# Kernel optimization log

Hardware: AMD Instinct MI355X
Metric: run time of the kernel (lower is better)

Reference implementation:

```python
import jax, jax.numpy as jnp
import numpy as np

DIM = 512
HEADS = 8
DIM_HEAD = 64
CROSS_DIM = 768
FF_INNER = 4 * DIM  # 2048
SCALE = DIM_HEAD ** -0.5
EPS = 1e-5


def _layer_norm(x, g, b):
    mu = jnp.mean(x, axis=-1, keepdims=True)
    var = jnp.var(x, axis=-1, keepdims=True)
    return (x - mu) * jax.lax.rsqrt(var + EPS) * g + b


def _mha(q, k, v):
    # q: [B,Sq,D], k/v: [B,Sk,D] -> [B,Sq,D]
    B, Sq, D = q.shape
    Sk = k.shape[1]
    qh = q.reshape(B, Sq, HEADS, DIM_HEAD).transpose(0, 2, 1, 3)
    kh = k.reshape(B, Sk, HEADS, DIM_HEAD).transpose(0, 2, 1, 3)
    vh = v.reshape(B, Sk, HEADS, DIM_HEAD).transpose(0, 2, 1, 3)
    scores = jnp.einsum('bhqd,bhkd->bhqk', qh, kh) * SCALE
    probs = jax.nn.softmax(scores, axis=-1)
    out = jnp.einsum('bhqk,bhkd->bhqd', probs, vh)
    return out.transpose(0, 2, 1, 3).reshape(B, Sq, D)


def setup_inputs() -> dict:
    key = jax.random.key(0)
    ks = jax.random.split(key, 20)
    s = 0.02
    inp = {
        'x': jax.random.normal(ks[0], (8, 1024, DIM), jnp.float32),
        'enc': jax.random.normal(ks[1], (8, 77, CROSS_DIM), jnp.float32),
        # self-attention (attn1)
        'ln1_g': jnp.ones((DIM,), jnp.float32),
        'ln1_b': jnp.zeros((DIM,), jnp.float32),
        'wq1': jax.random.normal(ks[2], (DIM, DIM), jnp.float32) * s,
        'wk1': jax.random.normal(ks[3], (DIM, DIM), jnp.float32) * s,
        'wv1': jax.random.normal(ks[4], (DIM, DIM), jnp.float32) * s,
        'wo1': jax.random.normal(ks[5], (DIM, DIM), jnp.float32) * s,
        'bo1': jnp.zeros((DIM,), jnp.float32),
        # cross-attention (attn2)
        'ln2_g': jnp.ones((DIM,), jnp.float32),
        'ln2_b': jnp.zeros((DIM,), jnp.float32),
        'wq2': jax.random.normal(ks[6], (DIM, DIM), jnp.float32) * s,
        'wk2': jax.random.normal(ks[7], (CROSS_DIM, DIM), jnp.float32) * s,
        'wv2': jax.random.normal(ks[8], (CROSS_DIM, DIM), jnp.float32) * s,
        'wo2': jax.random.normal(ks[9], (DIM, DIM), jnp.float32) * s,
        'bo2': jnp.zeros((DIM,), jnp.float32),
        # feed-forward (GEGLU)
        'ln3_g': jnp.ones((DIM,), jnp.float32),
        'ln3_b': jnp.zeros((DIM,), jnp.float32),
        'wg': jax.random.normal(ks[10], (DIM, 2 * FF_INNER), jnp.float32) * s,
        'bg': jnp.zeros((2 * FF_INNER,), jnp.float32),
        'wf': jax.random.normal(ks[11], (FF_INNER, DIM), jnp.float32) * s,
        'bf': jnp.zeros((DIM,), jnp.float32),
    }
    return inp


def reference(x, enc, ln1_g, ln1_b, wq1, wk1, wv1, wo1, bo1,
              ln2_g, ln2_b, wq2, wk2, wv2, wo2, bo2,
              ln3_g, ln3_b, wg, bg, wf, bf):
    # self-attention block (pre-norm)
    h = _layer_norm(x, ln1_g, ln1_b)
    a = _mha(h @ wq1, h @ wk1, h @ wv1)
    x = x + a @ wo1 + bo1
    # cross-attention block (pre-norm)
    h = _layer_norm(x, ln2_g, ln2_b)
    a = _mha(h @ wq2, enc @ wk2, enc @ wv2)
    x = x + a @ wo2 + bo2
    # GEGLU feed-forward (pre-norm)
    h = _layer_norm(x, ln3_g, ln3_b)
    proj = h @ wg + bg
    u, g = jnp.split(proj, 2, axis=-1)
    ff = (u * jax.nn.gelu(g, approximate=False)) @ wf + bf
    return x + ff
```

## Files before the change

### kernel.cpp

```cpp
#include <hip/hip_runtime.h>


typedef _Float16 half8 __attribute__((ext_vector_type(8)));
typedef float f32x4 __attribute__((ext_vector_type(4)));

__device__ __forceinline__ f32x4 mfma16(half8 a, half8 b, f32x4 c) {
  return __builtin_amdgcn_mfma_f32_16x16x32_f16(a, b, c, 0, 0, 0);
}

__device__ __forceinline__ void gload16(const _Float16* g, _Float16* l) {
  __builtin_amdgcn_global_load_lds(
      (const __attribute__((address_space(1))) void*)g,
      (__attribute__((address_space(3))) void*)l, 16, 0, 0);
}

struct PrepArgs {
  const float* src[10];
  _Float16* dst[10];
  int K[10], N[10], base[10];
  const float* enc;
  _Float16* ench;
  int encBase, nEnc;
};

__global__ __launch_bounds__(256)
void prep_all(PrepArgs pa) {
  __shared__ float tile[32][33];
  const int bid = blockIdx.x;
  const int tx = threadIdx.x, ty = threadIdx.y;
  if (bid >= pa.encBase) {
    const int i = (bid - pa.encBase) * 256 + ty * 32 + tx;
    if (i < pa.nEnc) pa.ench[i] = (_Float16)pa.enc[i];
    return;
  }
  int mi = 0;
  #pragma unroll
  for (int j = 1; j < 10; j++)
    if (bid >= pa.base[j]) mi = j;
  const int K = pa.K[mi], N = pa.N[mi];
  const int rel = bid - pa.base[mi];
  const int ntiles = N >> 5;
  const int bx = rel % ntiles, by = rel / ntiles;
  const float* src = pa.src[mi];
  _Float16* dst = pa.dst[mi];
  const int n0 = bx * 32, k0 = by * 32;
  #pragma unroll
  for (int j = ty; j < 32; j += 8)
    tile[j][tx] = src[(size_t)(k0 + j) * N + n0 + tx];
  __syncthreads();
  #pragma unroll
  for (int j = ty; j < 32; j += 8)
    dst[(size_t)(n0 + j) * K + k0 + tx] = (_Float16)tile[tx][j];
}

__global__ __launch_bounds__(256)
void vt_kernel(const _Float16* __restrict__ src, _Float16* __restrict__ dst,
               int S, int srcStride, int dstStride) {
  __shared__ _Float16 tile[32][33];
  const int tx = threadIdx.x, ty = threadIdx.y;
  const int s0 = blockIdx.x * 32, d0 = blockIdx.y * 32, bh = blockIdx.z;
  const int b = bh >> 3, h = bh & 7;
  const _Float16* sp = src + (size_t)b * S * srcStride + h * 64 + d0;
  #pragma unroll
  for (int j = ty; j < 32; j += 8) {
    int s = s0 + j; if (s >= S) s = S - 1;
    tile[j][tx] = sp[(size_t)s * srcStride + tx];
  }
  __syncthreads();
  _Float16* dp = dst + ((size_t)bh * 64 + d0) * dstStride + s0;
  #pragma unroll
  for (int j = ty; j < 32; j += 8)
    dp[(size_t)j * dstStride + tx] = tile[tx][j];
}

__global__ __launch_bounds__(256)
void ln_kernel(const float* __restrict__ x, const float* __restrict__ g,
               const float* __restrict__ b, _Float16* __restrict__ out) {
  const int row = blockIdx.x, t = threadIdx.x;
  const float* xr = x + (size_t)row * 512;
  float v0 = xr[t], v1 = xr[t + 256];
  float s1 = v0 + v1, s2 = v0 * v0 + v1 * v1;
  #pragma unroll
  for (int m = 32; m >= 1; m >>= 1) {
    s1 += __shfl_xor(s1, m);
    s2 += __shfl_xor(s2, m);
  }
  __shared__ float red[8];
  if ((t & 63) == 0) { red[t >> 6] = s1; red[4 + (t >> 6)] = s2; }
  __syncthreads();
  s1 = red[0] + red[1] + red[2] + red[3];
  s2 = red[4] + red[5] + red[6] + red[7];
  const float mu = s1 * (1.0f / 512.0f);
  const float var = s2 * (1.0f / 512.0f) - mu * mu;
  const float rs = rsqrtf(var + 1e-5f);
  out[(size_t)row * 512 + t] = (_Float16)((v0 - mu) * rs * g[t] + b[t]);
  out[(size_t)row * 512 + t + 256] =
      (_Float16)((v1 - mu) * rs * g[t + 256] + b[t + 256]);
}

template <int EPI, int GWM, int GWN, int WM, int WN, int MW, int SWZ>
__global__ __launch_bounds__(256, MW)
void gemm_bt(const _Float16* __restrict__ A, const _Float16* __restrict__ BT,
             int M, int N, int K, int lda, int ldc,
             _Float16* Ch, float* Cf,
             const float* __restrict__ bias, const float* resid) {
  constexpr int BM = GWM * WM * 16;
  constexpr int BN = GWN * WN * 16;
  __shared__ __align__(16) _Float16 As[2][4 * BM * 8];
  __shared__ __align__(16) _Float16 Bs[2][4 * BN * 8];
  __shared__ __align__(16) _Float16 Bs2[(EPI == 2) ? 2 : 1]
                                      [(EPI == 2) ? 4 * BN * 8 : 8];

  const int t = threadIdx.x;
  const int NNB = (N + BN - 1) / BN;
  int bm, bn;
  if constexpr (SWZ) {
    const int MG = (M / BM) >> 3;
    const int xcd = blockIdx.x & 7;
    const int s = blockIdx.x >> 3;
    bm = xcd * MG + s % MG;
    bn = s / MG;
  } else {
    bn = blockIdx.x % NNB;
    bm = blockIdx.x / NNB;
  }
  const int m0 = bm * BM, n0 = bn * BN;
  const int lane = t & 63, wv = t >> 6;
  const int quad = lane >> 4, l15 = lane & 15;
  const int wm = wv / GWN, wn = wv % GWN;

  f32x4 zero4 = {0.f, 0.f, 0.f, 0.f};
  f32x4 acc[WM][WN];
  f32x4 acc2[(EPI == 2) ? WM : 1][(EPI == 2) ? WN : 1];
  #pragma unroll
  for (int mi = 0; mi < WM; mi++)
    #pragma unroll
    for (int ni = 0; ni < WN; ni++) acc[mi][ni] = zero4;
  if constexpr (EPI == 2) {
    #pragma unroll
    for (int mi = 0; mi < WM; mi++)
      #pragma unroll
      for (int ni = 0; ni < WN; ni++) acc2[mi][ni] = zero4;
  }

  auto stageAll = [&](int k0, int pb) {
    #pragma unroll
    for (int c = wv; c < BM / 16; c += 4) {
      const int s = c * 64 + lane;
      const int q = s / BM;
      const int r = s % BM;
      int rg = m0 + r; if (rg >= M) rg = M - 1;
      gload16(A + (size_t)rg * lda + k0 + q * 8, &As[pb][c * 512]);
    }
    #pragma unroll
    for (int c = wv; c < BN / 16; c += 4) {
      const int s = c * 64 + lane;
      const int q = s / BN;
      const int r = s % BN;
      gload16(BT + (size_t)(n0 + r) * K + k0 + q * 8, &Bs[pb][c * 512]);
      if constexpr (EPI == 2)
        gload16(BT + (size_t)(2048 + n0 + r) * K + k0 + q * 8,
                &Bs2[pb][c * 512]);
    }
  };

  stageAll(0, 0);
  __syncthreads();

  const int NIT = K >> 5;
  for (int it = 0; it < NIT; ++it) {
    const int cur = it & 1;
    if (it + 1 < NIT) stageAll((it + 1) << 5, cur ^ 1);

    half8 fa[WM], fb[WN], fb2[(EPI == 2) ? WN : 1];
    #pragma unroll
    for (int mi = 0; mi < WM; mi++)
      fa[mi] = *(const half8*)(&As[cur]
          [((size_t)quad * BM + wm * WM * 16 + mi * 16 + l15) * 8]);
    #pragma unroll
    for (int ni = 0; ni < WN; ni++) {
      fb[ni] = *(const half8*)(&Bs[cur]
          [((size_t)quad * BN + wn * WN * 16 + ni * 16 + l15) * 8]);
      if constexpr (EPI == 2)
        fb2[ni] = *(const half8*)(&Bs2[cur]
            [((size_t)quad * BN + wn * WN * 16 + ni * 16 + l15) * 8]);
    }
    #pragma unroll
    for (int mi = 0; mi < WM; mi++)
      #pragma unroll
      for (int ni = 0; ni < WN; ni++) {
        acc[mi][ni] = mfma16(fa[mi], fb[ni], acc[mi][ni]);
        if constexpr (EPI == 2)
          acc2[mi][ni] = mfma16(fa[mi], fb2[ni], acc2[mi][ni]);
      }
    __syncthreads();
  }

  #pragma unroll
  for (int mi = 0; mi < WM; mi++) {
    const int rbase = m0 + wm * WM * 16 + mi * 16 + quad * 4;
    #pragma unroll
    for (int r = 0; r < 4; r++) {
      const int row = rbase + r;
      if (row >= M) continue;
      #pragma unroll
      for (int ni = 0; ni < WN; ni++) {
        const int col = n0 + wn * WN * 16 + ni * 16 + l15;
        const float v = acc[mi][ni][r];
        if constexpr (EPI == 0) {
          Ch[(size_t)row * ldc + col] = (_Float16)v;
        } else if constexpr (EPI == 1) {
          Cf[(size_t)row * ldc + col] =
              resid[(size_t)row * ldc + col] + v + bias[col];
        } else {
          const float u = v + bias[col];
          const float gg = acc2[mi][ni][r] + bias[col + 2048];
          const float ge = 0.5f * gg * (1.0f + erff(gg * 0.70710678118f));
          Ch[(size_t)row * ldc + col] = (_Float16)(u * ge);
        }
      }
    }
  }
}

__global__ __launch_bounds__(256)
void attn2(const _Float16* __restrict__ Q, const _Float16* __restrict__ K,
           const _Float16* __restrict__ VT, _Float16* __restrict__ O,
           int qStride, int kStride, long kBatchStride,
           int vtStride, int Sk) {
  __shared__ __align__(16) _Float16 KsL[2][2048];
  __shared__ __align__(16) _Float16 VTsL[2][2048];
  __shared__ __align__(16) _Float16 Ps[4][2][16][40];

  const int t = threadIdx.x;
  const int w = t >> 6, lane = t & 63, quad = lane >> 4, l15 = lane & 15;
  const int bh = blockIdx.y, b = bh >> 3, h = bh & 7;
  const int q0 = blockIdx.x * 128 + w * 32;

  const _Float16 qscale = (_Float16)(0.125f * 1.44269504f);
  half8 qf[2][2];
  #pragma unroll
  for (int mi = 0; mi < 2; mi++)
    #pragma unroll
    for (int c = 0; c < 2; c++) {
      const _Float16* qp = Q +
          (size_t)(b * 1024 + q0 + mi * 16 + l15) * qStride +
          h * 64 + c * 32 + quad * 8;
      half8 v = *(const half8*)qp;
      #pragma unroll
      for (int j = 0; j < 8; j++) v[j] *= qscale;
      qf[mi][c] = v;
    }

  f32x4 zero4 = {0.f, 0.f, 0.f, 0.f};
  f32x4 oa[2][4];
  float psum[2][4];
  #pragma unroll
  for (int mi = 0; mi < 2; mi++) {
    #pragma unroll
    for (int nt = 0; nt < 4; nt++) oa[mi][nt] = zero4;
    #pragma unroll
    for (int r = 0; r < 4; r++) psum[mi][r] = 0.f;
  }

  const _Float16* kp = K + (size_t)b * kBatchStride + h * 64;
  const _Float16* vtp = VT + (size_t)bh * 64 * vtStride;
  const int ksk = t & 31, kc = t >> 7, kqd = (t >> 5) & 3;
  const int vd = t & 63, vqd = t >> 6;

  auto stageKV = [&](int skb, int pb) {
    int skc = skb + ksk; if (skc >= Sk) skc = Sk - 1;
    gload16(kp + (size_t)skc * kStride + kc * 32 + kqd * 8, &KsL[pb][t * 8]);
    gload16(vtp + (size_t)vd * vtStride + skb + vqd * 8, &VTsL[pb][t * 8]);
  };

  stageKV(0, 0);
  __syncthreads();

  int it = 0;
  for (int skb = 0; skb < Sk; skb += 32, ++it) {
    const int cur = it & 1;
    if (skb + 32 < Sk) stageKV(skb + 32, cur ^ 1);

    const bool tail = (skb + 32 > Sk);
    #pragma unroll
    for (int mi = 0; mi < 2; mi++) {
      #pragma unroll
      for (int ct = 0; ct < 2; ct++) {
        f32x4 s = zero4;
        half8 kb0 = *(const half8*)(&KsL[cur][(quad * 32 + ct * 16 + l15) * 8]);
        half8 kb1 =
            *(const half8*)(&KsL[cur][(128 + quad * 32 + ct * 16 + l15) * 8]);
        s = mfma16(qf[mi][0], kb0, s);
        s = mfma16(qf[mi][1], kb1, s);
        if (tail) {
          const bool valid = (skb + ct * 16 + l15) < Sk;
          #pragma unroll
          for (int r = 0; r < 4; r++)
            if (!valid) s[r] = -__builtin_inff();
        }
        #pragma unroll
        for (int r = 0; r < 4; r++) {
          const float e = exp2f(s[r]);
          psum[mi][r] += e;
          Ps[w][mi][quad * 4 + r][ct * 16 + l15] = (_Float16)e;
        }
      }
    }
    #pragma unroll
    for (int mi = 0; mi < 2; mi++) {
      const half8 pf = *(const half8*)(&Ps[w][mi][l15][quad * 8]);
      #pragma unroll
      for (int nt = 0; nt < 4; nt++) {
        const half8 vf =
            *(const half8*)(&VTsL[cur][(quad * 64 + nt * 16 + l15) * 8]);
        oa[mi][nt] = mfma16(pf, vf, oa[mi][nt]);
      }
    }
    __syncthreads();
  }

  #pragma unroll
  for (int mi = 0; mi < 2; mi++)
    #pragma unroll
    for (int r = 0; r < 4; r++) {
      #pragma unroll
      for (int mm = 1; mm < 16; mm <<= 1)
        psum[mi][r] += __shfl_xor(psum[mi][r], mm);
      psum[mi][r] = 1.0f / psum[mi][r];
    }

  #pragma unroll
  for (int mi = 0; mi < 2; mi++)
    #pragma unroll
    for (int nt = 0; nt < 4; nt++)
      #pragma unroll
      for (int r = 0; r < 4; r++) {
        const size_t row = (size_t)(b * 1024 + q0 + mi * 16 + quad * 4 + r);
        O[row * 512 + h * 64 + nt * 16 + l15] =
            (_Float16)(oa[mi][nt][r] * psum[mi][r]);
      }
}

extern "C" void kernel_launch(void* const* d_in, const int* in_sizes, int n_in,
                              void* d_out, int out_size, void* d_ws,
                              size_t ws_size, hipStream_t stream) {
  const float* x    = (const float*)d_in[0];
  const float* enc  = (const float*)d_in[1];
  const float* ln1g = (const float*)d_in[2];
  const float* ln1b = (const float*)d_in[3];
  const float* wq1  = (const float*)d_in[4];
  const float* wk1  = (const float*)d_in[5];
  const float* wv1  = (const float*)d_in[6];
  const float* wo1  = (const float*)d_in[7];
  const float* bo1  = (const float*)d_in[8];
  const float* ln2g = (const float*)d_in[9];
  const float* ln2b = (const float*)d_in[10];
  const float* wq2  = (const float*)d_in[11];
  const float* wk2  = (const float*)d_in[12];
  const float* wv2  = (const float*)d_in[13];
  const float* wo2  = (const float*)d_in[14];
  const float* bo2  = (const float*)d_in[15];
  const float* ln3g = (const float*)d_in[16];
  const float* ln3b = (const float*)d_in[17];
  const float* wg   = (const float*)d_in[18];
  const float* bg   = (const float*)d_in[19];
  const float* wf   = (const float*)d_in[20];
  const float* bfp  = (const float*)d_in[21];
  float* out = (float*)d_out;

  char* ws = (char*)d_ws;
  _Float16* qkvT  = (_Float16*)(ws + 0);
  _Float16* q2T   = (_Float16*)(ws + 1572864);
  _Float16* kv2T  = (_Float16*)(ws + 2097152);
  _Float16* wo1T  = (_Float16*)(ws + 3670016);
  _Float16* wo2T  = (_Float16*)(ws + 4194304);
  _Float16* wgT   = (_Float16*)(ws + 4718592);
  _Float16* wfT   = (_Float16*)(ws + 8912896);
  _Float16* hbuf  = (_Float16*)(ws + 11010048);
  _Float16* qkv   = (_Float16*)(ws + 19398656);
  _Float16* q2b   = (_Float16*)(ws + 44564480);
  _Float16* kv2b  = (_Float16*)(ws + 52953088);
  _Float16* attnb = (_Float16*)(ws + 54214656);
  _Float16* ench  = (_Float16*)(ws + 62603264);
  _Float16* ffb   = (_Float16*)(ws + 19398656);
  _Float16* VTself = hbuf;
  _Float16* VTc    = ench;

  PrepArgs pa;
  const float* srcs[10] = {wq1, wk1, wv1, wo1, wq2, wk2, wv2, wo2, wg, wf};
  _Float16* dsts[10] = {qkvT, qkvT + 512 * 512, qkvT + 1024 * 512, wo1T, q2T,
                        kv2T, kv2T + 512 * 768, wo2T, wgT, wfT};
  const int Ks[10] = {512, 512, 512, 512, 512, 768, 768, 512, 512, 2048};
  const int Ns[10] = {512, 512, 512, 512, 512, 512, 512, 512, 4096, 512};
  int base = 0;
  for (int i = 0; i < 10; i++) {
    pa.src[i] = srcs[i]; pa.dst[i] = dsts[i];
    pa.K[i] = Ks[i]; pa.N[i] = Ns[i]; pa.base[i] = base;
    base += (Ks[i] >> 5) * (Ns[i] >> 5);
  }
  pa.enc = enc; pa.ench = ench; pa.encBase = base; pa.nEnc = 473088;
  const int prepBlocks = base + (473088 + 255) / 256;
  prep_all<<<prepBlocks, dim3(32, 8), 0, stream>>>(pa);

  const dim3 tb(32, 8);

  ln_kernel<<<8192, 256, 0, stream>>>(x, ln1g, ln1b, hbuf);
  gemm_bt<0, 2, 2, 4, 4, 2, 1><<<768, 256, 0, stream>>>(
      hbuf, qkvT, 8192, 1536, 512, 512, 1536, qkv, nullptr, nullptr, nullptr);
  vt_kernel<<<dim3(32, 2, 64), tb, 0, stream>>>(qkv + 1024, VTself, 1024, 1536, 1024);
  attn2<<<dim3(8, 64), 256, 0, stream>>>(qkv, qkv + 512, VTself, attnb,
                                         1536, 1536, (long)1024 * 1536,
                                         1024, 1024);
  gemm_bt<1, 1, 4, 4, 2, 3, 1><<<512, 256, 0, stream>>>(
      attnb, wo1T, 8192, 512, 512, 512, 512, nullptr, out, bo1, x);

  ln_kernel<<<8192, 256, 0, stream>>>(out, ln2g, ln2b, hbuf);
  gemm_bt<0, 1, 4, 4, 2, 3, 1><<<512, 256, 0, stream>>>(
      hbuf, q2T, 8192, 512, 512, 512, 512, q2b, nullptr, nullptr, nullptr);
  gemm_bt<0, 1, 4, 4, 2, 3, 0><<<80, 256, 0, stream>>>(
      ench, kv2T, 616, 1024, 768, 768, 1024, kv2b, nullptr, nullptr, nullptr);
  vt_kernel<<<dim3(3, 2, 64), tb, 0, stream>>>(kv2b + 512, VTc, 77, 1024, 96);
  attn2<<<dim3(8, 64), 256, 0, stream>>>(q2b, kv2b, VTc, attnb,
                                         512, 1024, (long)77 * 1024, 96, 77);
  gemm_bt<1, 1, 4, 4, 2, 3, 1><<<512, 256, 0, stream>>>(
      attnb, wo2T, 8192, 512, 512, 512, 512, nullptr, out, bo2, out);

  ln_kernel<<<8192, 256, 0, stream>>>(out, ln3g, ln3b, hbuf);
  gemm_bt<2, 2, 2, 4, 2, 2, 1><<<2048, 256, 0, stream>>>(
      hbuf, wgT, 8192, 2048, 512, 512, 2048, ffb, nullptr, bg, nullptr);
  gemm_bt<1, 1, 4, 4, 2, 3, 1><<<512, 256, 0, stream>>>(
      ffb, wfT, 8192, 512, 2048, 2048, 512, nullptr, out, bfp, out);
}
```

Before: 460.9 us.

## Replace LDS-staged block GEMM with per-wave direct-load GEMM on padded layouts

```diff
diff --git a/kernel.cpp b/kernel.cpp
--- a/kernel.cpp
+++ b/kernel.cpp
@@ -17,7 +17,7 @@
 struct PrepArgs {
   const float* src[10];
   _Float16* dst[10];
-  int K[10], N[10], base[10];
+  int K[10], N[10], base[10], ldT[10];
   const float* enc;
   _Float16* ench;
   int encBase, nEnc;
@@ -37,7 +37,7 @@
   #pragma unroll
   for (int j = 1; j < 10; j++)
     if (bid >= pa.base[j]) mi = j;
-  const int K = pa.K[mi], N = pa.N[mi];
+  const int N = pa.N[mi], ldT = pa.ldT[mi];
   const int rel = bid - pa.base[mi];
   const int ntiles = N >> 5;
   const int bx = rel % ntiles, by = rel / ntiles;
@@ -50,7 +50,7 @@
   __syncthreads();
   #pragma unroll
   for (int j = ty; j < 32; j += 8)
-    dst[(size_t)(n0 + j) * K + k0 + tx] = (_Float16)tile[tx][j];
+    dst[(size_t)(n0 + j) * ldT + k0 + tx] = (_Float16)tile[tx][j];
 }
 
 __global__ __launch_bounds__(256)
@@ -75,7 +75,8 @@
 
 __global__ __launch_bounds__(256)
 void ln_kernel(const float* __restrict__ x, const float* __restrict__ g,
-               const float* __restrict__ b, _Float16* __restrict__ out) {
+               const float* __restrict__ b, _Float16* __restrict__ out,
+               int ldo) {
   const int row = blockIdx.x, t = threadIdx.x;
   const float* xr = x + (size_t)row * 512;
   float v0 = xr[t], v1 = xr[t + 256];
@@ -93,41 +94,23 @@
   const float mu = s1 * (1.0f / 512.0f);
   const float var = s2 * (1.0f / 512.0f) - mu * mu;
   const float rs = rsqrtf(var + 1e-5f);
-  out[(size_t)row * 512 + t] = (_Float16)((v0 - mu) * rs * g[t] + b[t]);
-  out[(size_t)row * 512 + t + 256] =
+  out[(size_t)row * ldo + t] = (_Float16)((v0 - mu) * rs * g[t] + b[t]);
+  out[(size_t)row * ldo + t + 256] =
       (_Float16)((v1 - mu) * rs * g[t + 256] + b[t + 256]);
 }
 
-template <int EPI, int GWM, int GWN, int WM, int WN, int MW, int SWZ>
+template <int EPI, int WM, int WN, int MW>
 __global__ __launch_bounds__(256, MW)
-void gemm_bt(const _Float16* __restrict__ A, const _Float16* __restrict__ BT,
-             int M, int N, int K, int lda, int ldc,
-             _Float16* Ch, float* Cf,
-             const float* __restrict__ bias, const float* resid) {
-  constexpr int BM = GWM * WM * 16;
-  constexpr int BN = GWN * WN * 16;
-  __shared__ __align__(16) _Float16 As[2][4 * BM * 8];
-  __shared__ __align__(16) _Float16 Bs[2][4 * BN * 8];
-  __shared__ __align__(16) _Float16 Bs2[(EPI == 2) ? 2 : 1]
-                                      [(EPI == 2) ? 4 * BN * 8 : 8];
-
+void gemm_wave(const _Float16* __restrict__ A, const _Float16* __restrict__ BT,
+               int M, int NMT, int K, int lda, int ldb, int ldc,
+               _Float16* __restrict__ Ch, float* __restrict__ Cf,
+               const float* __restrict__ bias, const float* __restrict__ resid,
+               int dualOff) {
   const int t = threadIdx.x;
-  const int NNB = (N + BN - 1) / BN;
-  int bm, bn;
-  if constexpr (SWZ) {
-    const int MG = (M / BM) >> 3;
-    const int xcd = blockIdx.x & 7;
-    const int s = blockIdx.x >> 3;
-    bm = xcd * MG + s % MG;
-    bn = s / MG;
-  } else {
-    bn = blockIdx.x % NNB;
-    bm = blockIdx.x / NNB;
-  }
-  const int m0 = bm * BM, n0 = bn * BN;
-  const int lane = t & 63, wv = t >> 6;
-  const int quad = lane >> 4, l15 = lane & 15;
-  const int wm = wv / GWN, wn = wv % GWN;
+  const int lane = t & 63, quad = lane >> 4, l15 = lane & 15;
+  const int wid = blockIdx.x * 4 + (t >> 6);
+  const int bm = wid % NMT, bn = wid / NMT;
+  const int m0 = bm * (WM * 16), n0 = bn * (WN * 16);
 
   f32x4 zero4 = {0.f, 0.f, 0.f, 0.f};
   f32x4 acc[WM][WN];
@@ -143,80 +126,71 @@
       for (int ni = 0; ni < WN; ni++) acc2[mi][ni] = zero4;
   }
 
-  auto stageAll = [&](int k0, int pb) {
-    #pragma unroll
-    for (int c = wv; c < BM / 16; c += 4) {
-      const int s = c * 64 + lane;
-      const int q = s / BM;
-      const int r = s % BM;
-      int rg = m0 + r; if (rg >= M) rg = M - 1;
-      gload16(A + (size_t)rg * lda + k0 + q * 8, &As[pb][c * 512]);
-    }
-    #pragma unroll
-    for (int c = wv; c < BN / 16; c += 4) {
-      const int s = c * 64 + lane;
-      const int q = s / BN;
-      const int r = s % BN;
-      gload16(BT + (size_t)(n0 + r) * K + k0 + q * 8, &Bs[pb][c * 512]);
-      if constexpr (EPI == 2)
-        gload16(BT + (size_t)(2048 + n0 + r) * K + k0 + q * 8,
-                &Bs2[pb][c * 512]);
-    }
-  };
-
-  stageAll(0, 0);
-  __syncthreads();
-
-  const int NIT = K >> 5;
-  for (int it = 0; it < NIT; ++it) {
-    const int cur = it & 1;
-    if (it + 1 < NIT) stageAll((it + 1) << 5, cur ^ 1);
-
-    half8 fa[WM], fb[WN], fb2[(EPI == 2) ? WN : 1];
-    #pragma unroll
-    for (int mi = 0; mi < WM; mi++)
-      fa[mi] = *(const half8*)(&As[cur]
-          [((size_t)quad * BM + wm * WM * 16 + mi * 16 + l15) * 8]);
-    #pragma unroll
-    for (int ni = 0; ni < WN; ni++) {
-      fb[ni] = *(const half8*)(&Bs[cur]
-          [((size_t)quad * BN + wn * WN * 16 + ni * 16 + l15) * 8]);
-      if constexpr (EPI == 2)
-        fb2[ni] = *(const half8*)(&Bs2[cur]
-            [((size_t)quad * BN + wn * WN * 16 + ni * 16 + l15) * 8]);
-    }
-    #pragma unroll
-    for (int mi = 0; mi < WM; mi++)
+  const _Float16* ap[WM];
+  #pragma unroll
+  for (int mi = 0; mi < WM; mi++) {
+    int r = m0 + mi * 16 + l15; if (r >= M) r = M - 1;
+    ap[mi] = A + (size_t)r * lda + quad * 8;
+  }
+  const _Float16* bp[WN];
+  const _Float16* b2p[(EPI == 2) ? WN : 1];
+  #pragma unroll
+  for (int ni = 0; ni < WN; ni++) {
+    bp[ni] = BT + (size_t)(n0 + ni * 16 + l15) * ldb + quad * 8;
+    if constexpr (EPI == 2)
+      b2p[ni] = BT + (size_t)(dualOff + n0 + ni * 16 + l15) * ldb + quad * 8;
+  }
+
+  #pragma unroll 2
+  for (int k0 = 0; k0 < K; k0 += 64) {
+    half8 av[2][WM], bv[2][WN], b2v[2][(EPI == 2) ? WN : 1];
+    #pragma unroll
+    for (int kk = 0; kk < 2; kk++) {
+      #pragma unroll
+      for (int mi = 0; mi < WM; mi++)
+        av[kk][mi] = *(const half8*)(ap[mi] + k0 + kk * 32);
       #pragma unroll
       for (int ni = 0; ni < WN; ni++) {
-        acc[mi][ni] = mfma16(fa[mi], fb[ni], acc[mi][ni]);
+        bv[kk][ni] = *(const half8*)(bp[ni] + k0 + kk * 32);
         if constexpr (EPI == 2)
-          acc2[mi][ni] = mfma16(fa[mi], fb2[ni], acc2[mi][ni]);
+          b2v[kk][ni] = *(const half8*)(b2p[ni] + k0 + kk * 32);
       }
-    __syncthreads();
+    }
+    #pragma unroll
+    for (int kk = 0; kk < 2; kk++)
+      #pragma unroll
+      for (int mi = 0; mi < WM; mi++)
+        #pragma unroll
+        for (int ni = 0; ni < WN; ni++) {
+          acc[mi][ni] = mfma16(av[kk][mi], bv[kk][ni], acc[mi][ni]);
+          if constexpr (EPI == 2)
+            acc2[mi][ni] = mfma16(av[kk][mi], b2v[kk][ni], acc2[mi][ni]);
+        }
   }
 
   #pragma unroll
   for (int mi = 0; mi < WM; mi++) {
-    const int rbase = m0 + wm * WM * 16 + mi * 16 + quad * 4;
+    const int rbase = m0 + mi * 16 + quad * 4;
     #pragma unroll
     for (int r = 0; r < 4; r++) {
       const int row = rbase + r;
       if (row >= M) continue;
       #pragma unroll
       for (int ni = 0; ni < WN; ni++) {
-        const int col = n0 + wn * WN * 16 + ni * 16 + l15;
+        const int col = n0 + ni * 16 + l15;
         const float v = acc[mi][ni][r];
         if constexpr (EPI == 0) {
           Ch[(size_t)row * ldc + col] = (_Float16)v;
         } else if constexpr (EPI == 1) {
-          Cf[(size_t)row * ldc + col] =
-              resid[(size_t)row * ldc + col] + v + bias[col];
+          Cf[(size_t)row * 512 + col] =
+              resid[(size_t)row * 512 + col] + v + bias[col];
         } else {
           const float u = v + bias[col];
-          const float gg = acc2[mi][ni][r] + bias[col + 2048];
-          const float ge = 0.5f * gg * (1.0f + erff(gg * 0.70710678118f));
-          Ch[(size_t)row * ldc + col] = (_Float16)(u * ge);
+          const float gg = acc2[mi][ni][r] + bias[col + dualOff];
+          const float y = 0.7978845608f * (gg + 0.044715f * gg * gg * gg);
+          const float e = exp2f(2.885390082f * y);
+          const float th = (e - 1.0f) / (e + 1.0f);
+          Ch[(size_t)row * ldc + col] = (_Float16)(u * 0.5f * gg * (1.0f + th));
         }
       }
     }
@@ -227,7 +201,7 @@
 void attn2(const _Float16* __restrict__ Q, const _Float16* __restrict__ K,
            const _Float16* __restrict__ VT, _Float16* __restrict__ O,
            int qStride, int kStride, long kBatchStride,
-           int vtStride, int Sk) {
+           int vtStride, int Sk, int ldO) {
   __shared__ __align__(16) _Float16 KsL[2][2048];
   __shared__ __align__(16) _Float16 VTsL[2][2048];
   __shared__ __align__(16) _Float16 Ps[4][2][16][40];
@@ -337,7 +311,7 @@
       #pragma unroll
       for (int r = 0; r < 4; r++) {
         const size_t row = (size_t)(b * 1024 + q0 + mi * 16 + quad * 4 + r);
-        O[row * 512 + h * 64 + nt * 16 + l15] =
+        O[row * ldO + h * 64 + nt * 16 + l15] =
             (_Float16)(oa[mi][nt][r] * psum[mi][r]);
       }
 }
@@ -371,32 +345,33 @@
 
   char* ws = (char*)d_ws;
   _Float16* qkvT  = (_Float16*)(ws + 0);
-  _Float16* q2T   = (_Float16*)(ws + 1572864);
-  _Float16* kv2T  = (_Float16*)(ws + 2097152);
-  _Float16* wo1T  = (_Float16*)(ws + 3670016);
-  _Float16* wo2T  = (_Float16*)(ws + 4194304);
-  _Float16* wgT   = (_Float16*)(ws + 4718592);
-  _Float16* wfT   = (_Float16*)(ws + 8912896);
-  _Float16* hbuf  = (_Float16*)(ws + 11010048);
-  _Float16* qkv   = (_Float16*)(ws + 19398656);
-  _Float16* q2b   = (_Float16*)(ws + 44564480);
-  _Float16* kv2b  = (_Float16*)(ws + 52953088);
-  _Float16* attnb = (_Float16*)(ws + 54214656);
-  _Float16* ench  = (_Float16*)(ws + 62603264);
-  _Float16* ffb   = (_Float16*)(ws + 19398656);
+  _Float16* q2T   = (_Float16*)(ws + 1601536);
+  _Float16* kv2T  = (_Float16*)(ws + 2138112);
+  _Float16* wo1T  = (_Float16*)(ws + 3731456);
+  _Float16* wo2T  = (_Float16*)(ws + 4268032);
+  _Float16* wgT   = (_Float16*)(ws + 4804608);
+  _Float16* wfT   = (_Float16*)(ws + 9068544);
+  _Float16* hbuf  = (_Float16*)(ws + 11177984);
+  _Float16* qkv   = (_Float16*)(ws + 19701760);
+  _Float16* q2b   = (_Float16*)(ws + 44871680);
+  _Float16* kv2b  = (_Float16*)(ws + 53395456);
+  _Float16* attnb = (_Float16*)(ws + 54661120);
+  _Float16* ench  = q2b;
+  _Float16* ffb   = (_Float16*)(ws + 19701760);
   _Float16* VTself = hbuf;
-  _Float16* VTc    = ench;
+  _Float16* VTc    = kv2T;
 
   PrepArgs pa;
   const float* srcs[10] = {wq1, wk1, wv1, wo1, wq2, wk2, wv2, wo2, wg, wf};
-  _Float16* dsts[10] = {qkvT, qkvT + 512 * 512, qkvT + 1024 * 512, wo1T, q2T,
-                        kv2T, kv2T + 512 * 768, wo2T, wgT, wfT};
+  _Float16* dsts[10] = {qkvT, qkvT + 512 * 520, qkvT + 1024 * 520, wo1T, q2T,
+                        kv2T, kv2T + 512 * 776, wo2T, wgT, wfT};
   const int Ks[10] = {512, 512, 512, 512, 512, 768, 768, 512, 512, 2048};
   const int Ns[10] = {512, 512, 512, 512, 512, 512, 512, 512, 4096, 512};
   int base = 0;
   for (int i = 0; i < 10; i++) {
     pa.src[i] = srcs[i]; pa.dst[i] = dsts[i];
     pa.K[i] = Ks[i]; pa.N[i] = Ns[i]; pa.base[i] = base;
+    pa.ldT[i] = Ks[i] + 8;
     base += (Ks[i] >> 5) * (Ns[i] >> 5);
   }
   pa.enc = enc; pa.ench = ench; pa.encBase = base; pa.nEnc = 473088;
@@ -405,30 +380,36 @@
 
   const dim3 tb(32, 8);
 
-  ln_kernel<<<8192, 256, 0, stream>>>(x, ln1g, ln1b, hbuf);
-  gemm_bt<0, 2, 2, 4, 4, 2, 1><<<768, 256, 0, stream>>>(
-      hbuf, qkvT, 8192, 1536, 512, 512, 1536, qkv, nullptr, nullptr, nullptr);
-  vt_kernel<<<dim3(32, 2, 64), tb, 0, stream>>>(qkv + 1024, VTself, 1024, 1536, 1024);
+  ln_kernel<<<8192, 256, 0, stream>>>(x, ln1g, ln1b, hbuf, 520);
+  gemm_wave<0, 4, 4, 3><<<768, 256, 0, stream>>>(
+      hbuf, qkvT, 8192, 128, 512, 520, 520, 1536, qkv, nullptr, nullptr,
+      nullptr, 0);
+  vt_kernel<<<dim3(32, 2, 64), tb, 0, stream>>>(qkv + 1024, VTself, 1024,
+                                                1536, 1024);
   attn2<<<dim3(8, 64), 256, 0, stream>>>(qkv, qkv + 512, VTself, attnb,
                                          1536, 1536, (long)1024 * 1536,
-                                         1024, 1024);
-  gemm_bt<1, 1, 4, 4, 2, 3, 1><<<512, 256, 0, stream>>>(
-      attnb, wo1T, 8192, 512, 512, 512, 512, nullptr, out, bo1, x);
-
-  ln_kernel<<<8192, 256, 0, stream>>>(out, ln2g, ln2b, hbuf);
-  gemm_bt<0, 1, 4, 4, 2, 3, 1><<<512, 256, 0, stream>>>(
-      hbuf, q2T, 8192, 512, 512, 512, 512, q2b, nullptr, nullptr, nullptr);
-  gemm_bt<0, 1, 4, 4, 2, 3, 0><<<80, 256, 0, stream>>>(
-      ench, kv2T, 616, 1024, 768, 768, 1024, kv2b, nullptr, nullptr, nullptr);
+                                         1024, 1024, 520);
+  gemm_wave<1, 4, 4, 3><<<256, 256, 0, stream>>>(
+      attnb, wo1T, 8192, 128, 512, 520, 520, 512, nullptr, out, bo1, x, 0);
+
+  ln_kernel<<<8192, 256, 0, stream>>>(out, ln2g, ln2b, hbuf, 520);
+  gemm_wave<0, 4, 4, 3><<<40, 256, 0, stream>>>(
+      ench, kv2T, 616, 10, 768, 768, 776, 1024, kv2b, nullptr, nullptr,
+      nullptr, 0);
+  gemm_wave<0, 4, 4, 3><<<256, 256, 0, stream>>>(
+      hbuf, q2T, 8192, 128, 512, 520, 520, 520, q2b, nullptr, nullptr,
+      nullptr, 0);
   vt_kernel<<<dim3(3, 2, 64), tb, 0, stream>>>(kv2b + 512, VTc, 77, 1024, 96);
   attn2<<<dim3(8, 64), 256, 0, stream>>>(q2b, kv2b, VTc, attnb,
-                                         512, 1024, (long)77 * 1024, 96, 77);
-  gemm_bt<1, 1, 4, 4, 2, 3, 1><<<512, 256, 0, stream>>>(
-      attnb, wo2T, 8192, 512, 512, 512, 512, nullptr, out, bo2, out);
-
-  ln_kernel<<<8192, 256, 0, stream>>>(out, ln3g, ln3b, hbuf);
-  gemm_bt<2, 2, 2, 4, 2, 2, 1><<<2048, 256, 0, stream>>>(
-      hbuf, wgT, 8192, 2048, 512, 512, 2048, ffb, nullptr, bg, nullptr);
-  gemm_bt<1, 1, 4, 4, 2, 3, 1><<<512, 256, 0, stream>>>(
-      ffb, wfT, 8192, 512, 2048, 2048, 512, nullptr, out, bfp, out);
-}
+                                         520, 1024, (long)77 * 1024, 96, 77,
+                                         520);
+  gemm_wave<1, 4, 4, 3><<<256, 256, 0, stream>>>(
+      attnb, wo2T, 8192, 128, 512, 520, 520, 512, nullptr, out, bo2, out, 0);
+
+  ln_kernel<<<8192, 256, 0, stream>>>(out, ln3g, ln3b, hbuf, 520);
+  gemm_wave<2, 4, 2, 3><<<2048, 256, 0, stream>>>(
+      hbuf, wgT, 8192, 128, 512, 520, 520, 2056, ffb, nullptr, bg, nullptr,
+      2048);
+  gemm_wave<1, 4, 4, 3><<<256, 256, 0, stream>>>(
+      ffb, wfT, 8192, 128, 2048, 2056, 2056, 512, nullptr, out, bfp, out, 0);
+}
```

Result: slower. 536.8 us (+16.5%).

## Interleave GEGLU weight columns and retile output-projection GEMMs to 128x128

Applied to the files above, without the earlier changes.

```diff
diff --git a/kernel.cpp b/kernel.cpp
--- a/kernel.cpp
+++ b/kernel.cpp
@@ -17,7 +17,7 @@
 struct PrepArgs {
   const float* src[10];
   _Float16* dst[10];
-  int K[10], N[10], base[10];
+  int K[10], N[10], base[10], perm[10];
   const float* enc;
   _Float16* ench;
   int encBase, nEnc;
@@ -37,7 +37,7 @@
   #pragma unroll
   for (int j = 1; j < 10; j++)
     if (bid >= pa.base[j]) mi = j;
-  const int K = pa.K[mi], N = pa.N[mi];
+  const int K = pa.K[mi], N = pa.N[mi], pm = pa.perm[mi];
   const int rel = bid - pa.base[mi];
   const int ntiles = N >> 5;
   const int bx = rel % ntiles, by = rel / ntiles;
@@ -49,8 +49,11 @@
     tile[j][tx] = src[(size_t)(k0 + j) * N + n0 + tx];
   __syncthreads();
   #pragma unroll
-  for (int j = ty; j < 32; j += 8)
-    dst[(size_t)(n0 + j) * K + k0 + tx] = (_Float16)tile[tx][j];
+  for (int j = ty; j < 32; j += 8) {
+    int row = n0 + j;
+    if (pm) row = (row < 2048) ? (row * 2) : ((row - 2048) * 2 + 1);
+    dst[(size_t)row * K + k0 + tx] = (_Float16)tile[tx][j];
+  }
 }
 
 __global__ __launch_bounds__(256)
@@ -108,8 +111,6 @@
   constexpr int BN = GWN * WN * 16;
   __shared__ __align__(16) _Float16 As[2][4 * BM * 8];
   __shared__ __align__(16) _Float16 Bs[2][4 * BN * 8];
-  __shared__ __align__(16) _Float16 Bs2[(EPI == 2) ? 2 : 1]
-                                      [(EPI == 2) ? 4 * BN * 8 : 8];
 
   const int t = threadIdx.x;
   const int NNB = (N + BN - 1) / BN;
@@ -131,17 +132,10 @@
 
   f32x4 zero4 = {0.f, 0.f, 0.f, 0.f};
   f32x4 acc[WM][WN];
-  f32x4 acc2[(EPI == 2) ? WM : 1][(EPI == 2) ? WN : 1];
   #pragma unroll
   for (int mi = 0; mi < WM; mi++)
     #pragma unroll
     for (int ni = 0; ni < WN; ni++) acc[mi][ni] = zero4;
-  if constexpr (EPI == 2) {
-    #pragma unroll
-    for (int mi = 0; mi < WM; mi++)
-      #pragma unroll
-      for (int ni = 0; ni < WN; ni++) acc2[mi][ni] = zero4;
-  }
 
   auto stageAll = [&](int k0, int pb) {
     #pragma unroll
@@ -158,9 +152,6 @@
       const int q = s / BN;
       const int r = s % BN;
       gload16(BT + (size_t)(n0 + r) * K + k0 + q * 8, &Bs[pb][c * 512]);
-      if constexpr (EPI == 2)
-        gload16(BT + (size_t)(2048 + n0 + r) * K + k0 + q * 8,
-                &Bs2[pb][c * 512]);
     }
   };
 
@@ -172,27 +163,20 @@
     const int cur = it & 1;
     if (it + 1 < NIT) stageAll((it + 1) << 5, cur ^ 1);
 
-    half8 fa[WM], fb[WN], fb2[(EPI == 2) ? WN : 1];
+    half8 fa[WM], fb[WN];
     #pragma unroll
     for (int mi = 0; mi < WM; mi++)
       fa[mi] = *(const half8*)(&As[cur]
           [((size_t)quad * BM + wm * WM * 16 + mi * 16 + l15) * 8]);
     #pragma unroll
-    for (int ni = 0; ni < WN; ni++) {
+    for (int ni = 0; ni < WN; ni++)
       fb[ni] = *(const half8*)(&Bs[cur]
           [((size_t)quad * BN + wn * WN * 16 + ni * 16 + l15) * 8]);
-      if constexpr (EPI == 2)
-        fb2[ni] = *(const half8*)(&Bs2[cur]
-            [((size_t)quad * BN + wn * WN * 16 + ni * 16 + l15) * 8]);
-    }
     #pragma unroll
     for (int mi = 0; mi < WM; mi++)
       #pragma unroll
-      for (int ni = 0; ni < WN; ni++) {
+      for (int ni = 0; ni < WN; ni++)
         acc[mi][ni] = mfma16(fa[mi], fb[ni], acc[mi][ni]);
-        if constexpr (EPI == 2)
-          acc2[mi][ni] = mfma16(fa[mi], fb2[ni], acc2[mi][ni]);
-      }
     __syncthreads();
   }
 
@@ -202,21 +186,24 @@
     #pragma unroll
     for (int r = 0; r < 4; r++) {
       const int row = rbase + r;
-      if (row >= M) continue;
       #pragma unroll
       for (int ni = 0; ni < WN; ni++) {
         const int col = n0 + wn * WN * 16 + ni * 16 + l15;
         const float v = acc[mi][ni][r];
         if constexpr (EPI == 0) {
-          Ch[(size_t)row * ldc + col] = (_Float16)v;
+          if (row < M) Ch[(size_t)row * ldc + col] = (_Float16)v;
         } else if constexpr (EPI == 1) {
-          Cf[(size_t)row * ldc + col] =
-              resid[(size_t)row * ldc + col] + v + bias[col];
+          if (row < M)
+            Cf[(size_t)row * ldc + col] =
+                resid[(size_t)row * ldc + col] + v + bias[col];
         } else {
-          const float u = v + bias[col];
-          const float gg = acc2[mi][ni][r] + bias[col + 2048];
-          const float ge = 0.5f * gg * (1.0f + erff(gg * 0.70710678118f));
-          Ch[(size_t)row * ldc + col] = (_Float16)(u * ge);
+          const float vb = v + bias[(col >> 1) + ((col & 1) << 11)];
+          const float other = __shfl_xor(vb, 1);
+          if (!(col & 1) && row < M) {
+            const float gg = other;
+            const float ge = 0.5f * gg * (1.0f + erff(gg * 0.70710678118f));
+            Ch[(size_t)row * ldc + (col >> 1)] = (_Float16)(vb * ge);
+          }
         }
       }
     }
@@ -385,7 +372,8 @@
   _Float16* ench  = (_Float16*)(ws + 62603264);
   _Float16* ffb   = (_Float16*)(ws + 19398656);
   _Float16* VTself = hbuf;
-  _Float16* VTc    = ench;
+  _Float16* VTc    = kv2T;
+  VTc = (_Float16*)(ws + 62603264);
 
   PrepArgs pa;
   const float* srcs[10] = {wq1, wk1, wv1, wo1, wq2, wk2, wv2, wo2, wg, wf};
@@ -397,6 +385,7 @@
   for (int i = 0; i < 10; i++) {
     pa.src[i] = srcs[i]; pa.dst[i] = dsts[i];
     pa.K[i] = Ks[i]; pa.N[i] = Ns[i]; pa.base[i] = base;
+    pa.perm[i] = (i == 8) ? 1 : 0;
     base += (Ks[i] >> 5) * (Ns[i] >> 5);
   }
   pa.enc = enc; pa.ench = ench; pa.encBase = base; pa.nEnc = 473088;
@@ -408,27 +397,28 @@
   ln_kernel<<<8192, 256, 0, stream>>>(x, ln1g, ln1b, hbuf);
   gemm_bt<0, 2, 2, 4, 4, 2, 1><<<768, 256, 0, stream>>>(
       hbuf, qkvT, 8192, 1536, 512, 512, 1536, qkv, nullptr, nullptr, nullptr);
-  vt_kernel<<<dim3(32, 2, 64), tb, 0, stream>>>(qkv + 1024, VTself, 1024, 1536, 1024);
+  vt_kernel<<<dim3(32, 2, 64), tb, 0, stream>>>(qkv + 1024, VTself, 1024,
+                                                1536, 1024);
   attn2<<<dim3(8, 64), 256, 0, stream>>>(qkv, qkv + 512, VTself, attnb,
                                          1536, 1536, (long)1024 * 1536,
                                          1024, 1024);
-  gemm_bt<1, 1, 4, 4, 2, 3, 1><<<512, 256, 0, stream>>>(
+  gemm_bt<1, 2, 2, 4, 4, 2, 1><<<256, 256, 0, stream>>>(
       attnb, wo1T, 8192, 512, 512, 512, 512, nullptr, out, bo1, x);
 
   ln_kernel<<<8192, 256, 0, stream>>>(out, ln2g, ln2b, hbuf);
-  gemm_bt<0, 1, 4, 4, 2, 3, 1><<<512, 256, 0, stream>>>(
+  gemm_bt<0, 2, 2, 4, 4, 2, 1><<<256, 256, 0, stream>>>(
       hbuf, q2T, 8192, 512, 512, 512, 512, q2b, nullptr, nullptr, nullptr);
   gemm_bt<0, 1, 4, 4, 2, 3, 0><<<80, 256, 0, stream>>>(
       ench, kv2T, 616, 1024, 768, 768, 1024, kv2b, nullptr, nullptr, nullptr);
   vt_kernel<<<dim3(3, 2, 64), tb, 0, stream>>>(kv2b + 512, VTc, 77, 1024, 96);
   attn2<<<dim3(8, 64), 256, 0, stream>>>(q2b, kv2b, VTc, attnb,
                                          512, 1024, (long)77 * 1024, 96, 77);
-  gemm_bt<1, 1, 4, 4, 2, 3, 1><<<512, 256, 0, stream>>>(
+  gemm_bt<1, 2, 2, 4, 4, 2, 1><<<256, 256, 0, stream>>>(
       attnb, wo2T, 8192, 512, 512, 512, 512, nullptr, out, bo2, out);
 
   ln_kernel<<<8192, 256, 0, stream>>>(out, ln3g, ln3b, hbuf);
-  gemm_bt<2, 2, 2, 4, 2, 2, 1><<<2048, 256, 0, stream>>>(
-      hbuf, wgT, 8192, 2048, 512, 512, 2048, ffb, nullptr, bg, nullptr);
-  gemm_bt<1, 1, 4, 4, 2, 3, 1><<<512, 256, 0, stream>>>(
+  gemm_bt<3, 2, 2, 4, 4, 2, 1><<<2048, 256, 0, stream>>>(
+      hbuf, wgT, 8192, 4096, 512, 512, 2048, ffb, nullptr, bg, nullptr);
+  gemm_bt<1, 2, 2, 4, 4, 2, 1><<<256, 256, 0, stream>>>(
       ffb, wfT, 8192, 512, 2048, 2048, 512, nullptr, out, bfp, out);
 }
```

Result: slower. 499.3 us (+8.3%).
